# Performance work log

Hardware: AMD Instinct MI355X
Metric: run time of the kernel (lower is better)

The kernel has to match this reference:

```python
import jax, jax.numpy as jnp
import numpy as np
from jax import lax

PATCH_SIZE = 7
NEIGH_SIZE = 9
SIGMA = 2.0
EPS = 1e-05


def _gaussian_kernel(sigma, sz):
    mid = sz // 2
    ax = np.arange(sz) - mid
    g = np.exp(-(ax[:, None] ** 2 + ax[None, :] ** 2) / (2.0 * sigma ** 2)) / (2.0 * np.pi * sigma ** 2)
    return g.astype(np.float32)


KERNEL = jnp.asarray(_gaussian_kernel(SIGMA, PATCH_SIZE))[None, None]  # (1,1,7,7)

_half = NEIGH_SIZE // 2
SHIFTS = jnp.asarray(
    [(x, y) for x in range(-_half, NEIGH_SIZE - _half)
     for y in range(-_half, NEIGH_SIZE - _half) if (x, y) != (0, 0)],
    dtype=jnp.int32)  # (80, 2) — xshift outer loop, yshift inner, matching torch order
SHIFTS4 = jnp.asarray([(-1, 0), (1, 0), (0, -1), (0, 1)], dtype=jnp.int32)


def _translate(img, tx, ty):
    # Faithful to torch affine_grid + grid_sample(nearest, zeros, align_corners=False):
    # a 'translation' of tx in normalized coords samples input at pixel j + tx*W/2.
    # H, W even and tx, ty integers -> exact integer pixel shifts, zero padding.
    H, W = img.shape
    px = jnp.arange(W) + tx * (W // 2)
    py = jnp.arange(H) + ty * (H // 2)
    mask = ((py >= 0) & (py < H))[:, None] & ((px >= 0) & (px < W))[None, :]
    out = img[jnp.clip(py, 0, H - 1)[:, None], jnp.clip(px, 0, W - 1)[None, :]]
    return jnp.where(mask, out, jnp.zeros((), img.dtype))


def _blur(x):
    # x: (N, H, W); conv2d with gaussian kernel, stride 1, padding 3 (same for 7x7)
    y = lax.conv_general_dilated(x[:, None], KERNEL, (1, 1), [(3, 3), (3, 3)],
                                 dimension_numbers=('NCHW', 'OIHW', 'NCHW'))
    return y[:, 0]


def _dp_batch(img2d, shifts):
    # Dp for a batch of shifts: shift, diff, square, gaussian blur
    shifted = jax.vmap(lambda s: _translate(img2d, s[0], s[1]))(shifts)  # (N,H,W)
    return _blur((img2d[None] - shifted) ** 2)


def setup_inputs() -> dict:
    key = jax.random.key(0)
    k1, k2 = jax.random.split(key)
    image1 = jax.random.normal(k1, (1, 1, 1024, 1024), dtype=jnp.float32)
    image2 = jax.random.normal(k2, (1, 1, 1024, 1024), dtype=jnp.float32)
    return {"image1": image1, "image2": image2}


def reference(image1, image2):
    img1 = image1[0, 0]  # (H, W)
    img2 = image2[0, 0]
    H, W = img1.shape
    reduce_size = (PATCH_SIZE + NEIGH_SIZE - 2) // 2  # = 7
    # Vimg: average of 4 single-pixel-neighborhood Dp's on image1, + eps
    Vimg = _dp_batch(img1, SHIFTS4).sum(axis=0) / 4.0 + EPS  # (H, W)
    # 80-shift MIND responses on image2
    D2 = _dp_batch(img2, SHIFTS)  # (80, H, W)
    mind = jnp.exp(-D2 / Vimg[None])
    # torch slices: dim1 end index is (C - reduce_size) = 1-7 = -6 -> H-6;
    # dim2 end index is (H - reduce_size). Replicated exactly (H == W).
    out = mind[:, reduce_size:H + 1 - reduce_size, reduce_size:H - reduce_size]
    mx = jnp.max(out, axis=0)
    return jnp.mean(out / mx[None])
```

## Files before the change

### kernel.cpp

```cpp
#include <hip/hip_runtime.h>
#include <cmath>

#define IMG_W 1024
#define SROWS 22
#define SCOLS 70

struct GK { float gh[7]; float gv[7]; };

__device__ __forceinline__ float warp_block_sum(float v, float* wsum, int tx, int ty) {
    #pragma unroll
    for (int off = 32; off > 0; off >>= 1)
        v += __shfl_down(v, off, 64);
    if (tx == 0) wsum[ty] = v;
    __syncthreads();
    return wsum[0] + wsum[1] + wsum[2] + wsum[3];
}

__global__ __launch_bounds__(256)
void mind_tile(const float* __restrict__ img1, const float* __restrict__ img2,
               float* __restrict__ partials, GK gk)
{
    __shared__ float4 s1[SROWS * SCOLS];

    const int tx  = (int)threadIdx.x;
    const int ty  = (int)threadIdx.y;
    const int tid = ty * 64 + tx;
    const int x0  = 7 + 64 * (int)blockIdx.x;
    const int y0  = 7 + 16 * (int)blockIdx.y;

    #pragma unroll
    for (int k = 0; k < 7; ++k) {
        const int e = tid + 256 * k;
        if (e < SROWS * SCOLS) {
            const int r  = e / SCOLS;
            const int c  = e - r * SCOLS;
            const int sr = min(y0 - 3 + r, 1023);
            const int sc = min(x0 - 3 + c, 1023);
            const int srp = sr ^ 512;
            const int scp = sc ^ 512;
            const float a  = img2[sr  * IMG_W + sc ];
            const float b  = img2[sr  * IMG_W + scp];
            const float cc = img2[srp * IMG_W + sc ];
            const float d  = img2[srp * IMG_W + scp];
            const float u  = img1[sr  * IMG_W + sc ];
            const float ub = img1[sr  * IMG_W + scp];
            const float uc = img1[srp * IMG_W + sc ];
            const float a2 = a * a;
            const float tb = a - b, tc = a - cc, td = a - d;
            const float su = u - ub, sv = u - uc;
            float4 f;
            f.x = fmaf(tb, tb, -a2);
            f.y = fmaf(tc, tc, -a2);
            f.z = fmaf(td, td, -a2);
            f.w = fmaf(u, u + u, fmaf(su, su, sv * sv));
            s1[e] = f;
        }
    }
    __syncthreads();

    const bool xs = (x0 - 3 <= 511) && (x0 + 66 >= 512);
    const bool ys = (y0 - 3 <= 511) && (y0 + 18 >= 512);
    const bool xok = (x0 + tx <= 1016);
    float tsum = 0.f;

    if (!xs && !ys) {
        const bool xlo = ((x0 & 512) == 0);
        const bool ylo = ((y0 & 512) == 0);
        float Px[4] = {0,0,0,0}, Py[4] = {0,0,0,0}, Pd[4] = {0,0,0,0}, V4[4] = {0,0,0,0};
        #pragma unroll
        for (int r = 0; r < 10; ++r) {
            const float4* __restrict__ row = &s1[(4 * ty + r) * SCOLS + tx];
            float hH = 0, hV = 0, hD = 0, hU = 0;
            #pragma unroll
            for (int kx = 0; kx < 7; ++kx) {
                const float4 g = row[kx];
                hH = fmaf(gk.gh[kx], g.x, hH);
                hV = fmaf(gk.gh[kx], g.y, hV);
                hD = fmaf(gk.gh[kx], g.z, hD);
                hU = fmaf(gk.gh[kx], g.w, hU);
            }
            #pragma unroll
            for (int o = 0; o < 4; ++o) {
                if (r - o >= 0 && r - o <= 6) {
                    const float g = gk.gv[r - o];
                    Px[o] = fmaf(g, hH, Px[o]);
                    Py[o] = fmaf(g, hV, Py[o]);
                    Pd[o] = fmaf(g, hD, Pd[o]);
                    V4[o] = fmaf(g, hU, V4[o]);
                }
            }
        }
        (void)xlo; (void)ylo;
        #pragma unroll
        for (int o = 0; o < 4; ++o) {
            const float V = fmaf(V4[o], 0.25f, 1e-5f);
            const float invV = 1.0f / V;
            float M = fminf(0.f, Px[o]);
            M = fminf(M, Py[o]); M = fminf(M, Pd[o]);
            const float pix = 77.f * __expf(M * invV)
                + __expf((M - Px[o]) * invV)
                + __expf((M - Py[o]) * invV)
                + __expf((M - Pd[o]) * invV);
            const bool ok = xok && (y0 + 4 * ty + o <= 1017);
            tsum += ok ? pix : 0.f;
        }
    } else {
        float glx[7], ghx[7];
        #pragma unroll
        for (int kx = 0; kx < 7; ++kx) {
            const bool lo = (((x0 - 3 + tx + kx) & 512) == 0);
            glx[kx] = lo ? gk.gh[kx] : 0.f;
            ghx[kx] = lo ? 0.f : gk.gh[kx];
        }
        float Ph[4]  = {0,0,0,0}, Qh[4]  = {0,0,0,0}, Pv[4] = {0,0,0,0}, Qv[4] = {0,0,0,0};
        float Ppp[4] = {0,0,0,0}, Ppm[4] = {0,0,0,0}, Pmp[4] = {0,0,0,0}, Pmm[4] = {0,0,0,0};
        float V4[4]  = {0,0,0,0};
        #pragma unroll
        for (int r = 0; r < 10; ++r) {
            const float4* __restrict__ row = &s1[(4 * ty + r) * SCOLS + tx];
            float hHlo = 0, hHhi = 0, hV = 0, hDlo = 0, hDhi = 0, hU = 0;
            #pragma unroll
            for (int kx = 0; kx < 7; ++kx) {
                const float4 g = row[kx];
                hHlo = fmaf(glx[kx],   g.x, hHlo);
                hHhi = fmaf(ghx[kx],   g.x, hHhi);
                hV   = fmaf(gk.gh[kx], g.y, hV);
                hDlo = fmaf(glx[kx],   g.z, hDlo);
                hDhi = fmaf(ghx[kx],   g.z, hDhi);
                hU   = fmaf(gk.gh[kx], g.w, hU);
            }
            const bool ylo = (((y0 + 4 * ty - 3 + r) & 512) == 0);
            #pragma unroll
            for (int o = 0; o < 4; ++o) {
                if (r - o >= 0 && r - o <= 6) {
                    const float g  = gk.gv[r - o];
                    const float wl = ylo ? g : 0.f;
                    const float wh = ylo ? 0.f : g;
                    Ph [o] = fmaf(g,  hHlo, Ph [o]);
                    Qh [o] = fmaf(g,  hHhi, Qh [o]);
                    Pv [o] = fmaf(wl, hV,   Pv [o]);
                    Qv [o] = fmaf(wh, hV,   Qv [o]);
                    Ppp[o] = fmaf(wl, hDlo, Ppp[o]);
                    Ppm[o] = fmaf(wh, hDlo, Ppm[o]);
                    Pmp[o] = fmaf(wl, hDhi, Pmp[o]);
                    Pmm[o] = fmaf(wh, hDhi, Pmm[o]);
                    V4 [o] = fmaf(g,  hU,   V4 [o]);
                }
            }
        }
        #pragma unroll
        for (int o = 0; o < 4; ++o) {
            const float V = fmaf(V4[o], 0.25f, 1e-5f);
            const float invV = 1.0f / V;
            float M = fminf(0.f, Ph[o]);
            M = fminf(M, Qh[o]);  M = fminf(M, Pv[o]);  M = fminf(M, Qv[o]);
            M = fminf(M, Ppp[o]); M = fminf(M, Pmp[o]); M = fminf(M, Ppm[o]); M = fminf(M, Pmm[o]);
            const float pix = 72.f * __expf(M * invV)
                + __expf((M - Ph [o]) * invV) + __expf((M - Qh [o]) * invV)
                + __expf((M - Pv [o]) * invV) + __expf((M - Qv [o]) * invV)
                + __expf((M - Ppp[o]) * invV) + __expf((M - Pmp[o]) * invV)
                + __expf((M - Ppm[o]) * invV) + __expf((M - Pmm[o]) * invV);
            const bool ok = xok && (y0 + 4 * ty + o <= 1017);
            tsum += ok ? pix : 0.f;
        }
    }

    __shared__ float wsum[4];
    const float bt = warp_block_sum(tsum, wsum, tx, ty);
    if (tid == 0)
        partials[(int)blockIdx.y * gridDim.x + (int)blockIdx.x] = bt;
}

__global__ __launch_bounds__(256)
void mind_reduce(const float* __restrict__ partials, float* __restrict__ out)
{
    float s = 0.f;
    #pragma unroll
    for (int k = 0; k < 4; ++k)
        s += partials[(int)threadIdx.x + 256 * k];
    double d = (double)s;
    #pragma unroll
    for (int off = 32; off > 0; off >>= 1)
        d += __shfl_down(d, off, 64);
    __shared__ double sm[4];
    const int lane = (int)threadIdx.x & 63, wid = (int)threadIdx.x >> 6;
    if (lane == 0) sm[wid] = d;
    __syncthreads();
    if (threadIdx.x == 0)
        out[0] = (float)((sm[0] + sm[1] + sm[2] + sm[3]) / 81688800.0);
}

extern "C" void kernel_launch(void* const* d_in, const int* in_sizes, int n_in,
                              void* d_out, int out_size, void* d_ws, size_t ws_size,
                              hipStream_t stream) {
    const float* img1 = (const float*)d_in[0];
    const float* img2 = (const float*)d_in[1];
    float* out = (float*)d_out;
    float* partials = (float*)d_ws;

    GK gk;
    for (int i = 0; i < 7; ++i) {
        const double d = i - 3;
        gk.gh[i] = (float)std::exp(-(d * d) / 8.0);
        gk.gv[i] = (float)(std::exp(-(d * d) / 8.0) / (8.0 * M_PI));
    }

    dim3 block(64, 4);
    dim3 grid(16, 64);
    mind_tile<<<grid, block, 0, stream>>>(img1, img2, partials, gk);
    mind_reduce<<<1, 256, 0, stream>>>(partials, out);
}
```

Before: 71.98 us.

## Vectorize tile staging loads, pad shared rows, fuse final reduction into tile kernel

```diff
diff --git a/kernel.cpp b/kernel.cpp
--- a/kernel.cpp
+++ b/kernel.cpp
@@ -3,7 +3,7 @@
 
 #define IMG_W 1024
 #define SROWS 22
-#define SCOLS 70
+#define SCOLS 73
 
 struct GK { float gh[7]; float gv[7]; };
 
@@ -16,9 +16,10 @@
     return wsum[0] + wsum[1] + wsum[2] + wsum[3];
 }
 
-__global__ __launch_bounds__(256)
+__global__ __launch_bounds__(256, 4)
 void mind_tile(const float* __restrict__ img1, const float* __restrict__ img2,
-               float* __restrict__ partials, GK gk)
+               float* __restrict__ partials, int* __restrict__ counter,
+               float* __restrict__ out, GK gk)
 {
     __shared__ float4 s1[SROWS * SCOLS];
 
@@ -27,34 +28,39 @@
     const int tid = ty * 64 + tx;
     const int x0  = 7 + 64 * (int)blockIdx.x;
     const int y0  = 7 + 16 * (int)blockIdx.y;
-
-    #pragma unroll
-    for (int k = 0; k < 7; ++k) {
-        const int e = tid + 256 * k;
-        if (e < SROWS * SCOLS) {
-            const int r  = e / SCOLS;
-            const int c  = e - r * SCOLS;
-            const int sr = min(y0 - 3 + r, 1023);
-            const int sc = min(x0 - 3 + c, 1023);
-            const int srp = sr ^ 512;
-            const int scp = sc ^ 512;
-            const float a  = img2[sr  * IMG_W + sc ];
-            const float b  = img2[sr  * IMG_W + scp];
-            const float cc = img2[srp * IMG_W + sc ];
-            const float d  = img2[srp * IMG_W + scp];
-            const float u  = img1[sr  * IMG_W + sc ];
-            const float ub = img1[sr  * IMG_W + scp];
-            const float uc = img1[srp * IMG_W + sc ];
-            const float a2 = a * a;
-            const float tb = a - b, tc = a - cc, td = a - d;
-            const float su = u - ub, sv = u - uc;
-            float4 f;
-            f.x = fmaf(tb, tb, -a2);
-            f.y = fmaf(tc, tc, -a2);
-            f.z = fmaf(td, td, -a2);
-            f.w = fmaf(u, u + u, fmaf(su, su, sv * sv));
-            s1[e] = f;
-        }
+    const int x4  = x0 - 3;
+
+    #pragma unroll 2
+    for (int it = tid; it < SROWS * 18; it += 256) {
+        const int r   = it / 18;
+        const int j   = it - r * 18;
+        const int sr  = min(y0 - 3 + r, 1023);
+        const int srp = sr ^ 512;
+        const int scc = min(x4 + 4 * j, 1020);
+        const int scp = scc ^ 512;
+        const float4 a  = *(const float4*)&img2[sr  * IMG_W + scc];
+        const float4 b  = *(const float4*)&img2[sr  * IMG_W + scp];
+        const float4 c2 = *(const float4*)&img2[srp * IMG_W + scc];
+        const float4 d  = *(const float4*)&img2[srp * IMG_W + scp];
+        const float4 u  = *(const float4*)&img1[sr  * IMG_W + scc];
+        const float4 ub = *(const float4*)&img1[sr  * IMG_W + scp];
+        const float4 uc = *(const float4*)&img1[srp * IMG_W + scc];
+        float4* __restrict__ dst = &s1[r * SCOLS + 4 * j];
+        #define MIND_FIELD(E, K) { \
+            const float a2 = a.E * a.E; \
+            const float tb = a.E - b.E, tc = a.E - c2.E, td = a.E - d.E; \
+            const float su = u.E - ub.E, sv = u.E - uc.E; \
+            float4 f; \
+            f.x = fmaf(tb, tb, -a2);                            \
+            f.y = fmaf(tc, tc, -a2);                            \
+            f.z = fmaf(td, td, -a2);                            \
+            f.w = fmaf(u.E, u.E + u.E, fmaf(su, su, sv * sv));  \
+            dst[K] = f; }
+        MIND_FIELD(x, 0)
+        MIND_FIELD(y, 1)
+        MIND_FIELD(z, 2)
+        MIND_FIELD(w, 3)
+        #undef MIND_FIELD
     }
     __syncthreads();
 
@@ -167,27 +173,29 @@
 
     __shared__ float wsum[4];
     const float bt = warp_block_sum(tsum, wsum, tx, ty);
-    if (tid == 0)
-        partials[(int)blockIdx.y * gridDim.x + (int)blockIdx.x] = bt;
-}
-
-__global__ __launch_bounds__(256)
-void mind_reduce(const float* __restrict__ partials, float* __restrict__ out)
-{
-    float s = 0.f;
-    #pragma unroll
-    for (int k = 0; k < 4; ++k)
-        s += partials[(int)threadIdx.x + 256 * k];
-    double d = (double)s;
-    #pragma unroll
-    for (int off = 32; off > 0; off >>= 1)
-        d += __shfl_down(d, off, 64);
-    __shared__ double sm[4];
-    const int lane = (int)threadIdx.x & 63, wid = (int)threadIdx.x >> 6;
-    if (lane == 0) sm[wid] = d;
+    __shared__ int lastFlag;
+    if (tid == 0) {
+        partials[(int)blockIdx.y * 16 + (int)blockIdx.x] = bt;
+        __threadfence();
+        lastFlag = (atomicAdd(counter, 1) == 1023) ? 1 : 0;
+    }
     __syncthreads();
-    if (threadIdx.x == 0)
-        out[0] = (float)((sm[0] + sm[1] + sm[2] + sm[3]) / 81688800.0);
+    if (lastFlag) {
+        float s = 0.f;
+        #pragma unroll
+        for (int k = 0; k < 4; ++k)
+            s += __hip_atomic_load(&partials[tid + 256 * k],
+                                   __ATOMIC_RELAXED, __HIP_MEMORY_SCOPE_AGENT);
+        double dd = (double)s;
+        #pragma unroll
+        for (int off = 32; off > 0; off >>= 1)
+            dd += __shfl_down(dd, off, 64);
+        __shared__ double smd[4];
+        if (tx == 0) smd[ty] = dd;
+        __syncthreads();
+        if (tid == 0)
+            out[0] = (float)((smd[0] + smd[1] + smd[2] + smd[3]) / 81688800.0);
+    }
 }
 
 extern "C" void kernel_launch(void* const* d_in, const int* in_sizes, int n_in,
@@ -197,16 +205,17 @@
     const float* img2 = (const float*)d_in[1];
     float* out = (float*)d_out;
     float* partials = (float*)d_ws;
+    int* counter = (int*)((char*)d_ws + 4096);
 
     GK gk;
     for (int i = 0; i < 7; ++i) {
-        const double d = i - 3;
-        gk.gh[i] = (float)std::exp(-(d * d) / 8.0);
-        gk.gv[i] = (float)(std::exp(-(d * d) / 8.0) / (8.0 * M_PI));
-    }
-
+        const double dv = i - 3;
+        gk.gh[i] = (float)std::exp(-(dv * dv) / 8.0);
+        gk.gv[i] = (float)(std::exp(-(dv * dv) / 8.0) / (8.0 * M_PI));
+    }
+
+    hipMemsetAsync(counter, 0, sizeof(int), stream);
     dim3 block(64, 4);
     dim3 grid(16, 64);
-    mind_tile<<<grid, block, 0, stream>>>(img1, img2, partials, gk);
-    mind_reduce<<<1, 256, 0, stream>>>(partials, out);
+    mind_tile<<<grid, block, 0, stream>>>(img1, img2, partials, counter, out, gk);
 }
```

Result: slower. 106.9 us (+48.5%).
